# Performance work log

Measured on AMD Instinct MI355X. Metric: run time of the kernel, lower is better.

Reference implementation:

```python
import jax, jax.numpy as jnp
import numpy as np

D_MODEL = 1024
N_HEADS = 16
DK = D_MODEL // N_HEADS


def setup_inputs() -> dict:
    key = jax.random.key(0)
    ks = jax.random.split(key, 9)
    B, T = 4, 2048
    s = 1.0 / np.sqrt(D_MODEL)
    inp = {
        "x": jax.random.normal(ks[0], (B, T, D_MODEL), dtype=jnp.float32),
        "Wq": jax.random.normal(ks[1], (D_MODEL, D_MODEL), dtype=jnp.float32) * s,
        "bq": jnp.zeros((D_MODEL,), dtype=jnp.float32),
        "Wk": jax.random.normal(ks[2], (D_MODEL, D_MODEL), dtype=jnp.float32) * s,
        "bk": jnp.zeros((D_MODEL,), dtype=jnp.float32),
        "Wv": jax.random.normal(ks[3], (D_MODEL, D_MODEL), dtype=jnp.float32) * s,
        "bv": jnp.zeros((D_MODEL,), dtype=jnp.float32),
        "Wo": jax.random.normal(ks[4], (D_MODEL, D_MODEL), dtype=jnp.float32) * s,
        "bo": jnp.zeros((D_MODEL,), dtype=jnp.float32),
    }
    return inp


def reference(x, Wq, bq, Wk, bk, Wv, bv, Wo, bo):
    B, T, D = x.shape
    H, dk = N_HEADS, DK
    scale = 1.0 / np.sqrt(dk).astype(np.float32)

    def heads(t):  # [B,T,D] -> [B,H,T,dk]
        return t.reshape(B, T, H, dk).transpose(0, 2, 1, 3)

    Q = heads(x @ Wq + bq)
    K = heads(x @ Wk + bk)
    V = heads(x @ Wv + bv)
    scores = jnp.einsum("bhqd,bhkd->bhqk", Q, K) * scale
    attn = jax.nn.softmax(scores, axis=-1)  # dropout inactive at eval
    ctx = jnp.einsum("bhqk,bhkd->bhqd", attn, V)
    ctx = ctx.transpose(0, 2, 1, 3).reshape(B, T, D)
    return ctx @ Wo + bo
```

## Files before the change

kernel.cpp:

```cpp
#include <hip/hip_runtime.h>
#include <hip/hip_bf16.h>
#include <stdint.h>

#define D_MODEL 1024
#define NHEADS  16
#define DK      64
#define TSEQ    2048
#define BATCH   4
#define MROWS   8192

typedef __attribute__((ext_vector_type(8))) short bf16x8;
typedef __attribute__((ext_vector_type(4))) float f32x4;
typedef __attribute__((ext_vector_type(16))) float f32x16;

__device__ __forceinline__ void gl_lds16(const void* g, void* l) {
  __builtin_amdgcn_global_load_lds(
      (const __attribute__((address_space(1))) unsigned int*)g,
      (__attribute__((address_space(3))) unsigned int*)l,
      16, 0, 0);
}

__device__ __forceinline__ short f2bs(float f) {
  union { __hip_bfloat16 h; short s; } u;
  u.h = __float2bfloat16(f);
  return u.s;
}

__device__ __forceinline__ uint32_t cvt_pk(float lo, float hi) {
  uint32_t r;
  asm("s_nop 1\n\tv_cvt_pk_bf16_f32 %0, %1, %2" : "=v"(r) : "v"(lo), "v"(hi));
  return r;
}

__device__ __forceinline__ void permswap(uint32_t& a, uint32_t& b) {
  asm("v_permlane32_swap_b32 %0, %1" : "+v"(a), "+v"(b));
}

__global__ void cast_x_kernel(const float* __restrict__ in, short* __restrict__ out, int n4) {
  int i = blockIdx.x * blockDim.x + threadIdx.x;
  if (i >= n4) return;
  const float4 v = reinterpret_cast<const float4*>(in)[i];
  short4 r;
  r.x = f2bs(v.x); r.y = f2bs(v.y); r.z = f2bs(v.z); r.w = f2bs(v.w);
  reinterpret_cast<short4*>(out)[i] = r;
}

__global__ void transpose_cast4_kernel(
    const float* __restrict__ s0, const float* __restrict__ s1,
    const float* __restrict__ s2, const float* __restrict__ s3,
    short* __restrict__ d0, short* __restrict__ d1,
    short* __restrict__ d2, short* __restrict__ d3) {
  const int z = blockIdx.z;
  const float* src = (z == 0) ? s0 : (z == 1) ? s1 : (z == 2) ? s2 : s3;
  short* dst = (z == 0) ? d0 : (z == 1) ? d1 : (z == 2) ? d2 : d3;
  __shared__ float tile[32][33];
  const int tx = threadIdx.x, ty = threadIdx.y;
  const int n0 = blockIdx.x * 32, k0 = blockIdx.y * 32;
#pragma unroll
  for (int r = 0; r < 32; r += 8)
    tile[ty + r][tx] = src[(size_t)(k0 + ty + r) * D_MODEL + n0 + tx];
  __syncthreads();
#pragma unroll
  for (int r = 0; r < 32; r += 8)
    dst[(size_t)(n0 + ty + r) * D_MODEL + k0 + tx] = f2bs(tile[tx][ty + r]);
}

#define GEMM_MAIN_LOOP(A_, BT_)                                                     \
  __shared__ short SM[2][16384];              \
  const int tid = threadIdx.x;                                                      \
  const int lane = tid & 63;                                                        \
  const int w = tid >> 6;                                                           \
  const int wm = w >> 1, wn = w & 1;                                                \
  const int rowBase = blockIdx.x * 128;                                             \
  const int colBase = blockIdx.y * 128;                                             \
  const int g = lane >> 4;                                                          \
  const int c15 = lane & 15;                                                        \
  f32x4 acc[4][4];                                                                  \
  _Pragma("unroll")                                                                 \
  for (int i = 0; i < 4; ++i)                                                       \
    _Pragma("unroll")                                                               \
    for (int j = 0; j < 4; ++j) acc[i][j] = {0.f, 0.f, 0.f, 0.f};                   \
  const int srow = lane >> 3;                                                       \
  const int schunk8 = ((lane & 7) ^ srow) * 8;                                      \
  const short* gA = (A_) + (size_t)(rowBase + w * 32 + srow) * 1024 + schunk8;      \
  const short* gB = (BT_) + (size_t)(colBase + w * 32 + srow) * 1024 + schunk8;     \
  const int ko0 = ((g) ^ (c15 & 7)) * 8;                                            \
  const int ko1 = ((4 + g) ^ (c15 & 7)) * 8;                                        \
  _Pragma("unroll")                                                                 \
  for (int c = 0; c < 4; ++c) {                                                     \
    gl_lds16(gA + (size_t)(c * 8) * 1024, &SM[0][(w * 32 + c * 8) * 64]);           \
    gl_lds16(gB + (size_t)(c * 8) * 1024, &SM[0][8192 + (w * 32 + c * 8) * 64]);    \
  }                                                                                 \
  _Pragma("unroll 2")                                                               \
  for (int kt = 0; kt < 1024; kt += 64) {                                           \
    const int buf = (kt >> 6) & 1;                                                  \
    asm volatile("s_waitcnt vmcnt(0)" ::: "memory");                                \
    __builtin_amdgcn_s_barrier();                                                   \
    __builtin_amdgcn_sched_barrier(0);                                              \
    if (kt + 64 < 1024) {                                                           \
      _Pragma("unroll")                                                             \
      for (int c = 0; c < 4; ++c) {                                                 \
        gl_lds16(gA + (size_t)(c * 8) * 1024 + kt + 64, &SM[buf ^ 1][(w * 32 + c * 8) * 64]); \
        gl_lds16(gB + (size_t)(c * 8) * 1024 + kt + 64, &SM[buf ^ 1][8192 + (w * 32 + c * 8) * 64]); \
      }                                                                             \
    }                                                                               \
    const short* smA = &SM[buf][0];                                                 \
    const short* smB = &SM[buf][8192];                                              \
    bf16x8 af[4][2], bfr[4][2];                                                     \
    _Pragma("unroll")                                                               \
    for (int i = 0; i < 4; ++i) {                                                   \
      const int rb = (wm * 64 + i * 16 + c15) * 64;                                 \
      af[i][0] = *reinterpret_cast<const bf16x8*>(&smA[rb + ko0]);                  \
      af[i][1] = *reinterpret_cast<const bf16x8*>(&smA[rb + ko1]);                  \
    }                                                                               \
    _Pragma("unroll")                                                               \
    for (int j = 0; j < 4; ++j) {                                                   \
      const int rb = (wn * 64 + j * 16 + c15) * 64;                                 \
      bfr[j][0] = *reinterpret_cast<const bf16x8*>(&smB[rb + ko0]);                 \
      bfr[j][1] = *reinterpret_cast<const bf16x8*>(&smB[rb + ko1]);                 \
    }                                                                               \
    __builtin_amdgcn_s_setprio(1);                                                  \
    _Pragma("unroll")                                                               \
    for (int kk = 0; kk < 2; ++kk)                                                  \
      _Pragma("unroll")                                                             \
      for (int i = 0; i < 4; ++i)                                                   \
        _Pragma("unroll")                                                           \
        for (int j = 0; j < 4; ++j)                                                 \
          acc[i][j] = __builtin_amdgcn_mfma_f32_16x16x32_bf16(af[i][kk], bfr[j][kk], acc[i][j], 0, 0, 0); \
    __builtin_amdgcn_s_setprio(0);                                                  \
  }                                                                                 \
  __syncthreads();

__global__ __launch_bounds__(256, 2) void gemm_qkv_kernel(
    const short* __restrict__ A, const short* __restrict__ BTm,
    const float* __restrict__ bq, const float* __restrict__ bk,
    const float* __restrict__ bv, short* __restrict__ Qb,
    short* __restrict__ Kb, short* __restrict__ Vtb, float CL) {
  GEMM_MAIN_LOOP(A, BTm)
  const int mat = colBase >> 10;
  if (mat == 2) {
    short* smf = &SM[0][0];
    const int d_base = wn * 64 + c15;
#pragma unroll
    for (int j = 0; j < 4; ++j) {
      const int dl = d_base + j * 16;
      const int gcol = (colBase & 1023) + dl;
      const float bb = bv[gcol];
      const int sw = (dl & 15) << 3;
#pragma unroll
      for (int i = 0; i < 4; ++i) {
        const int tb = wm * 64 + i * 16 + g * 4;
#pragma unroll
        for (int r = 0; r < 4; r += 2) {
          const uint32_t p = cvt_pk(acc[i][j][r] + bb, acc[i][j][r + 1] + bb);
          *reinterpret_cast<uint32_t*>(&smf[dl * 128 + ((tb + r) ^ sw)]) = p;
        }
      }
    }
    __syncthreads();
    const int b0 = rowBase >> 11, t0 = rowBase & 2047;
    const int vcolBase = colBase & 1023;
#pragma unroll
    for (int k = 0; k < 8; ++k) {
      const int cid = k * 256 + tid;
      const int d = cid >> 4;
      const int c = cid & 15;
      const bf16x8 vv = *reinterpret_cast<const bf16x8*>(
          &smf[d * 128 + ((c * 8) ^ ((d & 15) << 3))]);
      *reinterpret_cast<bf16x8*>(
          &Vtb[((size_t)(b0 * 1024 + vcolBase + d)) * 2048 + t0 + c * 8]) = vv;
    }
  } else {
    const float* bp = (mat == 0) ? bq : bk;
    const float scl = (mat == 0) ? CL : 1.0f;
    short* Ob = (mat == 0) ? Qb : Kb;
#pragma unroll
    for (int i = 0; i < 4; ++i) {
#pragma unroll
      for (int j = 0; j < 4; ++j) {
#pragma unroll
        for (int r = 0; r < 4; ++r) {
          const int grow = rowBase + wm * 64 + i * 16 + g * 4 + r;
          const int gcol = (colBase + wn * 64 + j * 16 + c15) & 1023;
          const float v = (acc[i][j][r] + bp[gcol]) * scl;
          const int b = grow >> 11, t = grow & 2047;
          const int h = gcol >> 6, d = gcol & 63;
          Ob[((size_t)(b * NHEADS + h) * TSEQ + t) * DK + d] = f2bs(v);
        }
      }
    }
  }
}

__global__ __launch_bounds__(256, 2) void gemm_out_kernel(
    const short* __restrict__ A, const short* __restrict__ BTm,
    const float* __restrict__ bias, float* __restrict__ Cout) {
  GEMM_MAIN_LOOP(A, BTm)
#pragma unroll
  for (int i = 0; i < 4; ++i) {
#pragma unroll
    for (int j = 0; j < 4; ++j) {
#pragma unroll
      for (int r = 0; r < 4; ++r) {
        const int grow = rowBase + wm * 64 + i * 16 + g * 4 + r;
        const int gcol = colBase + wn * 64 + j * 16 + c15;
        Cout[(size_t)grow * 1024 + gcol] = acc[i][j][r] + bias[gcol];
      }
    }
  }
}

__global__ __launch_bounds__(256, 4) void attn_kernel(
    const short* __restrict__ Qg, const short* __restrict__ Kg,
    const short* __restrict__ Vtg, short* __restrict__ ctx) {
  __shared__ short Ks[2][64 * 64];
  __shared__ short VTs[2][64 * 64];

  const int tid = threadIdx.x;
  const int lane = tid & 63;
  const int w = tid >> 6;
  const int l5 = lane >> 5;
  const int c31 = lane & 31;
  const int lid = blockIdx.x;
  const int bh = (lid >> 7) * 8 + (lid & 7);
  const int qbase = ((lid >> 3) & 15) * 128;
  const int b = bh >> 4, h = bh & 15;

  const short* Qp = Qg + (size_t)bh * TSEQ * DK;
  const short* Kp = Kg + (size_t)bh * TSEQ * DK;
  const short* Vtp = Vtg + (size_t)bh * DK * TSEQ;

  const int qrow = qbase + w * 32 + c31;

  bf16x8 qf[4];
#pragma unroll
  for (int kd = 0; kd < 4; ++kd)
    qf[kd] = *reinterpret_cast<const bf16x8*>(Qp + (size_t)qrow * DK + kd * 16 + l5 * 8);

  f32x16 o0, o1;
#pragma unroll
  for (int r = 0; r < 16; ++r) { o0[r] = 0.f; o1[r] = 0.f; }
  float l_s = 0.f;

  f32x16 z16;
#pragma unroll
  for (int r = 0; r < 16; ++r) z16[r] = 0.f;

  const int srow = w * 8 + (lane >> 3);
  const int soff = ((lane & 7) ^ (lane >> 3) ^ (w & 3)) * 8;
  const int swz = (((c31 & 7) ^ (c31 >> 3)) << 4);

  int offA[4];
#pragma unroll
  for (int kd = 0; kd < 4; ++kd)
    offA[kd] = c31 * 64 + ((((kd * 32 + l5 * 16)) ^ swz) >> 1);

#define STAGE(T, SLOT) do {                                                          \
    const int kt_ = (T) * 64;                                                        \
    _Pragma("unroll")                                                                \
    for (int c = 0; c < 2; ++c) {                                                    \
      const int row_ = c * 32 + srow;                                                \
      gl_lds16(Kp + (size_t)(kt_ + row_) * DK + soff, &Ks[SLOT][(c * 4 + w) * 512]); \
      gl_lds16(Vtp + (size_t)row_ * TSEQ + kt_ + soff, &VTs[SLOT][(c * 4 + w) * 512]); \
    }                                                                                \
  } while (0)

#define BODY(T, SLOT, PREFETCH) do {                                                 \
    asm volatile("s_waitcnt vmcnt(0)" ::: "memory");                                 \
    __builtin_amdgcn_s_barrier();                                                    \
    __builtin_amdgcn_sched_barrier(0);                                               \
    if (PREFETCH) STAGE((T) + 1, (SLOT) ^ 1);                                        \
    const short* ksb = &Ks[SLOT][0];                                                 \
    const short* vtb = &VTs[SLOT][0];                                                \
    __builtin_amdgcn_s_setprio(1);                                                   \
    const bf16x8 kf0a = *reinterpret_cast<const bf16x8*>(ksb + offA[0]);             \
    const bf16x8 kf1a = *reinterpret_cast<const bf16x8*>(ksb + 2048 + offA[0]);      \
    f32x16 s0 = __builtin_amdgcn_mfma_f32_32x32x16_bf16(kf0a, qf[0], z16, 0, 0, 0);  \
    f32x16 s1 = __builtin_amdgcn_mfma_f32_32x32x16_bf16(kf1a, qf[0], z16, 0, 0, 0);  \
    _Pragma("unroll")                                                                \
    for (int kd = 1; kd < 4; ++kd) {                                                 \
      const bf16x8 kf0 = *reinterpret_cast<const bf16x8*>(ksb + offA[kd]);           \
      const bf16x8 kf1 = *reinterpret_cast<const bf16x8*>(ksb + 2048 + offA[kd]);    \
      s0 = __builtin_amdgcn_mfma_f32_32x32x16_bf16(kf0, qf[kd], s0, 0, 0, 0);        \
      s1 = __builtin_amdgcn_mfma_f32_32x32x16_bf16(kf1, qf[kd], s1, 0, 0, 0);        \
    }                                                                                \
    __builtin_amdgcn_s_setprio(0);                                                   \
    float p0 = 0.f, p1 = 0.f, p2 = 0.f, p3 = 0.f;                                    \
    _Pragma("unroll")                                                                \
    for (int r = 0; r < 16; r += 4) {                                                \
      s0[r] = __builtin_amdgcn_exp2f(s0[r]);                                         \
      s0[r + 1] = __builtin_amdgcn_exp2f(s0[r + 1]);                                 \
      s0[r + 2] = __builtin_amdgcn_exp2f(s0[r + 2]);                                 \
      s0[r + 3] = __builtin_amdgcn_exp2f(s0[r + 3]);                                 \
      p0 += s0[r]; p1 += s0[r + 1]; p2 += s0[r + 2]; p3 += s0[r + 3];                \
    }                                                                                \
    _Pragma("unroll")                                                                \
    for (int r = 0; r < 16; r += 4) {                                                \
      s1[r] = __builtin_amdgcn_exp2f(s1[r]);                                         \
      s1[r + 1] = __builtin_amdgcn_exp2f(s1[r + 1]);                                 \
      s1[r + 2] = __builtin_amdgcn_exp2f(s1[r + 2]);                                 \
      s1[r + 3] = __builtin_amdgcn_exp2f(s1[r + 3]);                                 \
      p0 += s1[r]; p1 += s1[r + 1]; p2 += s1[r + 2]; p3 += s1[r + 3];                \
    }                                                                                \
    l_s += (p0 + p1) + (p2 + p3);                                                    \
    uint32_t wa[8], wb[8];                                                           \
    _Pragma("unroll")                                                                \
    for (int t2 = 0; t2 < 8; ++t2) {                                                 \
      wa[t2] = cvt_pk(s0[2 * t2], s0[2 * t2 + 1]);                                   \
      wb[t2] = cvt_pk(s1[2 * t2], s1[2 * t2 + 1]);                                   \
    }                                                                                \
    permswap(wa[0], wa[2]); permswap(wa[1], wa[3]);                                  \
    permswap(wa[4], wa[6]); permswap(wa[5], wa[7]);                                  \
    permswap(wb[0], wb[2]); permswap(wb[1], wb[3]);                                  \
    permswap(wb[4], wb[6]); permswap(wb[5], wb[7]);                                  \
    bf16x8 pf[4];                                                                    \
    {                                                                                \
      union { uint32_t u[4]; bf16x8 v; } fr;                                         \
      fr.u[0] = wa[0]; fr.u[1] = wa[1]; fr.u[2] = wa[2]; fr.u[3] = wa[3]; pf[0] = fr.v; \
      fr.u[0] = wa[4]; fr.u[1] = wa[5]; fr.u[2] = wa[6]; fr.u[3] = wa[7]; pf[1] = fr.v; \
      fr.u[0] = wb[0]; fr.u[1] = wb[1]; fr.u[2] = wb[2]; fr.u[3] = wb[3]; pf[2] = fr.v; \
      fr.u[0] = wb[4]; fr.u[1] = wb[5]; fr.u[2] = wb[6]; fr.u[3] = wb[7]; pf[3] = fr.v; \
    }                                                                                \
    __builtin_amdgcn_s_setprio(1);                                                   \
    _Pragma("unroll")                                                                \
    for (int ks = 0; ks < 4; ++ks) {                                                 \
      const bf16x8 vf0 = *reinterpret_cast<const bf16x8*>(vtb + offA[ks]);           \
      const bf16x8 vf1 = *reinterpret_cast<const bf16x8*>(vtb + 2048 + offA[ks]);    \
      o0 = __builtin_amdgcn_mfma_f32_32x32x16_bf16(vf0, pf[ks], o0, 0, 0, 0);        \
      o1 = __builtin_amdgcn_mfma_f32_32x32x16_bf16(vf1, pf[ks], o1, 0, 0, 0);        \
    }                                                                                \
    __builtin_amdgcn_s_setprio(0);                                                   \
  } while (0)

  STAGE(0, 0);
  for (int t = 0; t < 30; t += 2) {
    BODY(t, 0, true);
    BODY(t + 1, 1, true);
  }
  BODY(30, 0, true);
  BODY(31, 1, false);

#undef STAGE
#undef BODY

  l_s += __shfl_xor(l_s, 32, 64);

  const float inv = 1.0f / l_s;
  short* crow = ctx + ((size_t)b * TSEQ + qrow) * D_MODEL + h * 64;
#pragma unroll
  for (int r = 0; r < 16; ++r) {
    const int d = (r & 3) + 8 * (r >> 2) + 4 * l5;
    crow[d] = f2bs(o0[r] * inv);
    crow[32 + d] = f2bs(o1[r] * inv);
  }
}

extern "C" void kernel_launch(void* const* d_in, const int* in_sizes, int n_in,
                              void* d_out, int out_size, void* d_ws, size_t ws_size,
                              hipStream_t stream) {
  const float* x  = (const float*)d_in[0];
  const float* Wq = (const float*)d_in[1];
  const float* bq = (const float*)d_in[2];
  const float* Wk = (const float*)d_in[3];
  const float* bk = (const float*)d_in[4];
  const float* Wv = (const float*)d_in[5];
  const float* bv = (const float*)d_in[6];
  const float* Wo = (const float*)d_in[7];
  const float* bo = (const float*)d_in[8];
  float* out = (float*)d_out;

  short* xb   = (short*)d_ws;
  short* WqT  = xb + (size_t)MROWS * D_MODEL;
  short* WkT  = WqT + (size_t)D_MODEL * D_MODEL;
  short* WvT  = WkT + (size_t)D_MODEL * D_MODEL;
  short* WoT  = WvT + (size_t)D_MODEL * D_MODEL;
  short* Qb   = WoT + (size_t)D_MODEL * D_MODEL;
  short* Kb   = Qb + (size_t)MROWS * D_MODEL;
  short* Vtb  = Kb + (size_t)MROWS * D_MODEL;
  short* ctxb = xb;

  const float CL = 0.1803368801111204f;

  cast_x_kernel<<<(MROWS * D_MODEL / 4 + 255) / 256, 256, 0, stream>>>(x, xb, MROWS * D_MODEL / 4);
  transpose_cast4_kernel<<<dim3(32, 32, 4), dim3(32, 8), 0, stream>>>(
      Wq, Wk, Wv, Wo, WqT, WkT, WvT, WoT);

  gemm_qkv_kernel<<<dim3(MROWS / 128, 3 * D_MODEL / 128), 256, 0, stream>>>(
      xb, WqT, bq, bk, bv, Qb, Kb, Vtb, CL);

  attn_kernel<<<1024, 256, 0, stream>>>(Qb, Kb, Vtb, ctxb);

  gemm_out_kernel<<<dim3(MROWS / 128, D_MODEL / 128), 256, 0, stream>>>(ctxb, WoT, bo, out);
}
```

Before: 167.4 us.

## Merge prep kernels, split K/V waitcnts in attention, pack ctx stores

Merges the x cast and the weight transpose-cast into one launch with an extended grid, which removes one kernel launch. In the attention loop, K loads are issued before V loads. The wait at the top of each iteration now covers only K (vmcnt(2)), and a second wait before the PV MFMAs covers V, so V loading overlaps QK and softmax. The ctx epilogue writes packed pairs of bf16 with cvt_pk instead of single shorts. The gains depend on launch overhead and on memory latency inside the attention loop; the wait counts are tied to the exact number of loads each thread issues.

```diff
diff --git a/kernel.cpp b/kernel.cpp
--- a/kernel.cpp
+++ b/kernel.cpp
@@ -36,33 +36,38 @@
   asm("v_permlane32_swap_b32 %0, %1" : "+v"(a), "+v"(b));
 }
 
-__global__ void cast_x_kernel(const float* __restrict__ in, short* __restrict__ out, int n4) {
-  int i = blockIdx.x * blockDim.x + threadIdx.x;
-  if (i >= n4) return;
-  const float4 v = reinterpret_cast<const float4*>(in)[i];
-  short4 r;
-  r.x = f2bs(v.x); r.y = f2bs(v.y); r.z = f2bs(v.z); r.w = f2bs(v.w);
-  reinterpret_cast<short4*>(out)[i] = r;
-}
-
-__global__ void transpose_cast4_kernel(
+__global__ void prep_kernel(
+    const float* __restrict__ x, short* __restrict__ xb,
     const float* __restrict__ s0, const float* __restrict__ s1,
     const float* __restrict__ s2, const float* __restrict__ s3,
     short* __restrict__ d0, short* __restrict__ d1,
     short* __restrict__ d2, short* __restrict__ d3) {
   const int z = blockIdx.z;
-  const float* src = (z == 0) ? s0 : (z == 1) ? s1 : (z == 2) ? s2 : s3;
-  short* dst = (z == 0) ? d0 : (z == 1) ? d1 : (z == 2) ? d2 : d3;
-  __shared__ float tile[32][33];
-  const int tx = threadIdx.x, ty = threadIdx.y;
-  const int n0 = blockIdx.x * 32, k0 = blockIdx.y * 32;
-#pragma unroll
-  for (int r = 0; r < 32; r += 8)
-    tile[ty + r][tx] = src[(size_t)(k0 + ty + r) * D_MODEL + n0 + tx];
-  __syncthreads();
-#pragma unroll
-  for (int r = 0; r < 32; r += 8)
-    dst[(size_t)(n0 + ty + r) * D_MODEL + k0 + tx] = f2bs(tile[tx][ty + r]);
+  if (z < 4) {
+    const float* src = (z == 0) ? s0 : (z == 1) ? s1 : (z == 2) ? s2 : s3;
+    short* dst = (z == 0) ? d0 : (z == 1) ? d1 : (z == 2) ? d2 : d3;
+    __shared__ float tile[32][33];
+    const int tx = threadIdx.x, ty = threadIdx.y;
+    const int n0 = blockIdx.x * 32, k0 = blockIdx.y * 32;
+#pragma unroll
+    for (int r = 0; r < 32; r += 8)
+      tile[ty + r][tx] = src[(size_t)(k0 + ty + r) * D_MODEL + n0 + tx];
+    __syncthreads();
+#pragma unroll
+    for (int r = 0; r < 32; r += 8)
+      dst[(size_t)(n0 + ty + r) * D_MODEL + k0 + tx] = f2bs(tile[tx][ty + r]);
+  } else {
+    const int c = (z - 4) * 1024 + blockIdx.y * 32 + blockIdx.x;
+    const int base = (c * 256 + (int)(threadIdx.y * 32 + threadIdx.x)) * 2;
+#pragma unroll
+    for (int q = 0; q < 2; ++q) {
+      const int i = base + q;
+      const float4 v = reinterpret_cast<const float4*>(x)[i];
+      short4 r;
+      r.x = f2bs(v.x); r.y = f2bs(v.y); r.z = f2bs(v.z); r.w = f2bs(v.w);
+      reinterpret_cast<short4*>(xb)[i] = r;
+    }
+  }
 }
 
 #define GEMM_MAIN_LOOP(A_, BT_)                                                     \
@@ -261,12 +266,16 @@
     for (int c = 0; c < 2; ++c) {                                                    \
       const int row_ = c * 32 + srow;                                                \
       gl_lds16(Kp + (size_t)(kt_ + row_) * DK + soff, &Ks[SLOT][(c * 4 + w) * 512]); \
+    }                                                                                \
+    _Pragma("unroll")                                                                \
+    for (int c = 0; c < 2; ++c) {                                                    \
+      const int row_ = c * 32 + srow;                                                \
       gl_lds16(Vtp + (size_t)row_ * TSEQ + kt_ + soff, &VTs[SLOT][(c * 4 + w) * 512]); \
     }                                                                                \
   } while (0)
 
 #define BODY(T, SLOT, PREFETCH) do {                                                 \
-    asm volatile("s_waitcnt vmcnt(0)" ::: "memory");                                 \
+    asm volatile("s_waitcnt vmcnt(2)" ::: "memory");                \
     __builtin_amdgcn_s_barrier();                                                    \
     __builtin_amdgcn_sched_barrier(0);                                               \
     if (PREFETCH) STAGE((T) + 1, (SLOT) ^ 1);                                        \
@@ -321,6 +330,7 @@
       fr.u[0] = wb[0]; fr.u[1] = wb[1]; fr.u[2] = wb[2]; fr.u[3] = wb[3]; pf[2] = fr.v; \
       fr.u[0] = wb[4]; fr.u[1] = wb[5]; fr.u[2] = wb[6]; fr.u[3] = wb[7]; pf[3] = fr.v; \
     }                                                                                \
+    asm volatile("s_waitcnt vmcnt(%0)" :: "i"((PREFETCH) ? 4 : 0) : "memory");       \
     __builtin_amdgcn_s_setprio(1);                                                   \
     _Pragma("unroll")                                                                \
     for (int ks = 0; ks < 4; ++ks) {                                                 \
@@ -348,10 +358,10 @@
   const float inv = 1.0f / l_s;
   short* crow = ctx + ((size_t)b * TSEQ + qrow) * D_MODEL + h * 64;
 #pragma unroll
-  for (int r = 0; r < 16; ++r) {
+  for (int r = 0; r < 16; r += 2) {
     const int d = (r & 3) + 8 * (r >> 2) + 4 * l5;
-    crow[d] = f2bs(o0[r] * inv);
-    crow[32 + d] = f2bs(o1[r] * inv);
+    *reinterpret_cast<uint32_t*>(&crow[d]) = cvt_pk(o0[r] * inv, o0[r + 1] * inv);
+    *reinterpret_cast<uint32_t*>(&crow[32 + d]) = cvt_pk(o1[r] * inv, o1[r + 1] * inv);
   }
 }
 
@@ -381,9 +391,8 @@
 
   const float CL = 0.1803368801111204f;
 
-  cast_x_kernel<<<(MROWS * D_MODEL / 4 + 255) / 256, 256, 0, stream>>>(x, xb, MROWS * D_MODEL / 4);
-  transpose_cast4_kernel<<<dim3(32, 32, 4), dim3(32, 8), 0, stream>>>(
-      Wq, Wk, Wv, Wo, WqT, WkT, WvT, WoT);
+  prep_kernel<<<dim3(32, 32, 8), dim3(32, 8), 0, stream>>>(
+      x, xb, Wq, Wk, Wv, Wo, WqT, WkT, WvT, WoT);
 
   gemm_qkv_kernel<<<dim3(MROWS / 128, 3 * D_MODEL / 128), 256, 0, stream>>>(
       xb, WqT, bq, bk, bv, Qb, Kb, Vtb, CL);
```

Result: no change. 164.2 us (-1.9%).
